# Kernel tuning notes

Measured on AMD Instinct MI355X. Metric: run time of the kernel, lower is better.

## Reference

```python
import jax, jax.numpy as jnp
import numpy as np

NEG_INF = -9e15
ALPHA = 0.2  # LeakyReLU negative slope


def setup_inputs() -> dict:
    key = jax.random.key(0)
    k1, k2, k3, k4 = jax.random.split(key, 4)
    B, N, C_IN, C_OUT, H = 8, 2048, 256, 256, 4
    node_feats = jax.random.normal(k1, (B, N, C_IN), dtype=jnp.float32)
    adj_matrix = jax.random.randint(k2, (B, N, N), 0, 2, dtype=jnp.int32)
    # include self-connections as the docstring expects
    eye = jnp.eye(N, dtype=jnp.int32)[None]
    adj_matrix = jnp.maximum(adj_matrix, eye)
    W = jax.random.normal(k3, (C_OUT, C_IN), dtype=jnp.float32) * (1.414 / np.sqrt(C_IN))
    b = jnp.zeros((C_OUT,), dtype=jnp.float32)
    a = jax.random.normal(k4, (H, 2 * (C_OUT // H)), dtype=jnp.float32) * 0.1
    return {"node_feats": node_feats, "adj_matrix": adj_matrix, "W": W, "b": b, "a": a}


def reference(node_feats, adj_matrix, W, b, a):
    B, N, _ = node_feats.shape
    H, two_c = a.shape
    c = two_c // 2
    # projection: [B, N, H, c]
    f = (jnp.einsum('bni,oi->bno', node_feats, W) + b).reshape(B, N, H, c)
    # attention logit for edge (i, j): leakyrelu(a . [f_i, f_j])
    # decomposes as leakyrelu(s_src[i] + s_dst[j])
    a_src, a_dst = a[:, :c], a[:, c:]
    s_src = jnp.einsum('bnhc,hc->bnh', f, a_src)  # [B, N, H]
    s_dst = jnp.einsum('bnhc,hc->bnh', f, a_dst)  # [B, N, H]
    logits = jax.nn.leaky_relu(s_src[:, :, None, :] + s_dst[:, None, :, :], ALPHA)  # [B,N,N,H]
    logits = jnp.where(adj_matrix[..., None] == 1, logits, NEG_INF)
    probs = jax.nn.softmax(logits, axis=2)  # softmax over source nodes j
    out = jnp.einsum('bijh,bjhc->bihc', probs, f)
    return out.reshape(B, N, H * c)  # concat_heads=True
```

## Files before the change

kernel.cpp:

```cpp
#include <hip/hip_runtime.h>

#define LOG2E 1.4426950408889634f

typedef __attribute__((ext_vector_type(8))) short short8;
typedef __attribute__((ext_vector_type(4))) float f32x4;

union AF { unsigned u[4]; short8 v; };
union BB { uint4 q; short8 v; };

__device__ __forceinline__ unsigned short f2bf(float f) {
  unsigned int u = __float_as_uint(f);
  u = (u + 0x7fffu + ((u >> 16) & 1u)) >> 16;
  return (unsigned short)u;
}

__global__ __launch_bounds__(256) void gat_k1(
    const float* __restrict__ X, const float* __restrict__ W,
    const float* __restrict__ bias, const float* __restrict__ a,
    unsigned short* __restrict__ ft, float* __restrict__ ssrc,
    float* __restrict__ sdst)
{
  __shared__ float Xs[8][128];
  __shared__ float Ws[8][128];
  const int tid = threadIdx.x;
  const int tx = tid & 15, ty = tid >> 4;
  const int m0 = blockIdx.x * 128;
  const int c0 = blockIdx.y * 128;

  float acc[8][8];
#pragma unroll
  for (int r = 0; r < 8; ++r)
#pragma unroll
    for (int j = 0; j < 8; ++j) acc[r][j] = 0.f;

  const int lrow = tid >> 1;
  const int kk0 = (tid & 1) * 4;
  const float* Xp = X + (size_t)(m0 + lrow) * 256 + kk0;
  const float* Wp = W + (size_t)(c0 + lrow) * 256 + kk0;

  for (int kc = 0; kc < 256; kc += 8) {
    float4 xv = *(const float4*)(Xp + kc);
    float4 wv = *(const float4*)(Wp + kc);
    __syncthreads();
    Xs[kk0 + 0][lrow] = xv.x; Xs[kk0 + 1][lrow] = xv.y;
    Xs[kk0 + 2][lrow] = xv.z; Xs[kk0 + 3][lrow] = xv.w;
    Ws[kk0 + 0][lrow] = wv.x; Ws[kk0 + 1][lrow] = wv.y;
    Ws[kk0 + 2][lrow] = wv.z; Ws[kk0 + 3][lrow] = wv.w;
    __syncthreads();
#pragma unroll
    for (int kk = 0; kk < 8; ++kk) {
      float av[8], wv8[8];
#pragma unroll
      for (int r = 0; r < 8; ++r) av[r] = Xs[kk][ty * 8 + r];
#pragma unroll
      for (int j = 0; j < 8; ++j) wv8[j] = Ws[kk][tx * 8 + j];
#pragma unroll
      for (int r = 0; r < 8; ++r)
#pragma unroll
        for (int j = 0; j < 8; ++j) acc[r][j] = fmaf(av[r], wv8[j], acc[r][j]);
    }
  }

  const int b = m0 >> 11;
  const int nloc0 = (m0 & 2047) + ty * 8;
  const int cg0 = c0 + tx * 8;
  const int h = cg0 >> 6;
  const int cb = cg0 & 63;

  float bv[8], av_s[8], av_d[8];
#pragma unroll
  for (int j = 0; j < 8; ++j) {
    bv[j]   = bias[cg0 + j];
    av_s[j] = a[h * 128 + cb + j];
    av_d[j] = a[h * 128 + 64 + cb + j];
  }
#pragma unroll
  for (int r = 0; r < 8; ++r)
#pragma unroll
    for (int j = 0; j < 8; ++j) acc[r][j] += bv[j];

  const int jt = nloc0 >> 4;
  const int ni = nloc0 & 15;
#pragma unroll
  for (int j = 0; j < 8; ++j) {
    unsigned int u[4];
#pragma unroll
    for (int q = 0; q < 4; ++q) {
      unsigned int lo = f2bf(acc[2 * q + 0][j]);
      unsigned int hi = f2bf(acc[2 * q + 1][j]);
      u[q] = lo | (hi << 16);
    }
    size_t off = ((((size_t)b * 128 + jt) * 4 + h) * 64 + (cb + j)) * 16 + ni;
    *(uint4*)(ft + off) = make_uint4(u[0], u[1], u[2], u[3]);
  }

  float sp[8], dp[8];
#pragma unroll
  for (int r = 0; r < 8; ++r) {
    float s = 0.f, d = 0.f;
#pragma unroll
    for (int j = 0; j < 8; ++j) {
      s = fmaf(acc[r][j], av_s[j], s);
      d = fmaf(acc[r][j], av_d[j], d);
    }
    sp[r] = s; dp[r] = d;
  }
#pragma unroll
  for (int off = 1; off < 8; off <<= 1) {
#pragma unroll
    for (int r = 0; r < 8; ++r) {
      sp[r] += __shfl_xor(sp[r], off);
      dp[r] += __shfl_xor(dp[r], off);
    }
  }
  if ((tx & 7) == 0) {
    float* sb = ssrc + ((size_t)b * 4 + h) * 2048 + nloc0;
    float* db = sdst + ((size_t)b * 4 + h) * 2048 + nloc0;
#pragma unroll
    for (int r = 0; r < 8; ++r) { sb[r] = sp[r] * LOG2E; db[r] = dp[r] * LOG2E; }
  }
}

__global__ __launch_bounds__(512, 5) void gat_k2(
    const int* __restrict__ adj, const unsigned short* __restrict__ ft,
    const float* __restrict__ ssrc, const float* __restrict__ sdst,
    float* __restrict__ out)
{
  __shared__ __align__(16) unsigned char lds[37120];
  float* sd = (float*)lds;
  unsigned* Aw = (unsigned*)(lds + 32768);

  const int tid = threadIdx.x;
  const int b = blockIdx.x & 7;
  const int itile = blockIdx.x >> 3;
  const int i0 = itile * 16;
  const int w = tid >> 6;
  const int h = w >> 1;
  const int p = w & 1;
  const int lane = tid & 63;
  const int i_l = lane & 15;
  const int kg = lane >> 4;
  const int shamt = kg * 8;

  const unsigned short* ftb =
      ft + ((((size_t)b * 128 + p * 64 + (kg >> 1)) * 4 + h) * 64 + i_l) * 16 +
      (kg & 1) * 8;

  uint4 A0, A1, A2, A3, B0, B1, B2, B3;
#define LOADB(s, P0_, P1_, P2_, P3_)                               \
  {                                                                \
    const unsigned short* fp_ = ftb + (size_t)(s) * 8192;          \
    P0_ = *(const uint4*)(fp_);                                    \
    P1_ = *(const uint4*)(fp_ + 256);                              \
    P2_ = *(const uint4*)(fp_ + 512);                              \
    P3_ = *(const uint4*)(fp_ + 768);                              \
  }
  LOADB(0, A0, A1, A2, A3)
  LOADB(1, B0, B1, B2, B3)

  {
    const float4* src = (const float4*)(sdst + (size_t)b * 4 * 2048);
    float4* dst = (float4*)sd;
#pragma unroll
    for (int q = 0; q < 4; ++q) dst[tid + q * 512] = src[tid + q * 512];
  }
  {
    const int* abase = adj + (size_t)b * 2048 * 2048 + (size_t)i0 * 2048;
    unsigned short* dst16 = (unsigned short*)Aw;
#pragma unroll
    for (int k = 0; k < 4; ++k) {
      const int idx = k * 512 + tid;
      const int r = idx >> 7;
      const int s16 = idx & 127;
      const int4* ap = (const int4*)(abase + (size_t)r * 2048 + s16 * 16);
      int4 v0 = ap[0], v1 = ap[1], v2 = ap[2], v3 = ap[3];
      int vv[16] = {v0.x, v0.y, v0.z, v0.w, v1.x, v1.y, v1.z, v1.w,
                    v2.x, v2.y, v2.z, v2.w, v3.x, v3.y, v3.z, v3.w};
      unsigned m = 0;
#pragma unroll
      for (int i = 0; i < 16; ++i) m |= (vv[i] ? 1u : 0u) << i;
      dst16[((s16 >> 1) * 17 + r) * 2 + (s16 & 1)] = (unsigned short)m;
    }
  }
  const float si = ssrc[((size_t)b * 4 + h) * 2048 + i0 + i_l];
  const float* sdh = sd + h * 2048 + p * 1024 + kg * 8;

  f32x4 acc0, acc1, acc2, acc3;
#pragma unroll
  for (int q = 0; q < 4; ++q) { acc0[q] = 0.f; acc1[q] = 0.f; acc2[q] = 0.f; acc3[q] = 0.f; }
  float lsumA = 0.f, lsumB = 0.f;

  __syncthreads();

#define LOADM(s, mw_, t0_, t1_)                                    \
  {                                                                \
    mw_ = Aw[(p * 32 + (s)) * 17 + i_l];                           \
    const float* tp_ = sdh + (size_t)(s) * 32;                     \
    t0_ = *(const float4*)tp_;                                     \
    t1_ = *(const float4*)(tp_ + 4);                               \
  }

#define COMPE(mw_, t0_, t1_, af_, lsum_)                           \
  {                                                                \
    const unsigned byte_ = ((mw_) >> shamt) & 0xffu;               \
    float tj_[8] = {t0_.x, t0_.y, t0_.z, t0_.w,                    \
                    t1_.x, t1_.y, t1_.z, t1_.w};                   \
    float e_[8];                                                   \
    _Pragma("unroll")                                              \
    for (int q = 0; q < 8; ++q) {                                  \
      float x_ = si + tj_[q];                                      \
      float y_ = fmaxf(x_, 0.2f * x_);                             \
      float ev_ = __builtin_amdgcn_exp2f(y_);                      \
      e_[q] = (byte_ & (1u << q)) ? ev_ : 0.f;                     \
    }                                                              \
    float s01_ = e_[0] + e_[1], s23_ = e_[2] + e_[3];              \
    float s45_ = e_[4] + e_[5], s67_ = e_[6] + e_[7];              \
    lsum_ += (s01_ + s23_) + (s45_ + s67_);                        \
    _Pragma("unroll")                                              \
    for (int q2 = 0; q2 < 4; ++q2) {                               \
      unsigned r_;                                                 \
      asm("v_cvt_pk_bf16_f32 %0, %1, %2"                           \
          : "=v"(r_) : "v"(e_[2 * q2]), "v"(e_[2 * q2 + 1]));      \
      af_.u[q2] = r_;                                              \
    }                                                              \
  }

#define DOMFMA(af_, P0_, P1_, P2_, P3_)                            \
  {                                                                \
    BB bb_;                                                        \
    bb_.q = P0_;                                                   \
    acc0 = __builtin_amdgcn_mfma_f32_16x16x32_bf16(af_.v, bb_.v, acc0, 0, 0, 0); \
    bb_.q = P1_;                                                   \
    acc1 = __builtin_amdgcn_mfma_f32_16x16x32_bf16(af_.v, bb_.v, acc1, 0, 0, 0); \
    bb_.q = P2_;                                                   \
    acc2 = __builtin_amdgcn_mfma_f32_16x16x32_bf16(af_.v, bb_.v, acc2, 0, 0, 0); \
    bb_.q = P3_;                                                   \
    acc3 = __builtin_amdgcn_mfma_f32_16x16x32_bf16(af_.v, bb_.v, acc3, 0, 0, 0); \
  }

  unsigned mwA, mwB;
  float4 ta0, ta1, tb0, tb1;
  LOADM(0, mwA, ta0, ta1)

  for (int s = 0; s < 32; s += 2) {
    LOADM(s + 1, mwB, tb0, tb1)
    AF afA;
    COMPE(mwA, ta0, ta1, afA, lsumA)
    DOMFMA(afA, A0, A1, A2, A3)
    {
      const int sn = (s + 2 < 32) ? s + 2 : 31;
      LOADB(sn, A0, A1, A2, A3)
    }
    {
      const int sm = (s + 2 < 32) ? s + 2 : 31;
      LOADM(sm, mwA, ta0, ta1)
    }
    AF afB;
    COMPE(mwB, tb0, tb1, afB, lsumB)
    DOMFMA(afB, B0, B1, B2, B3)
    {
      const int sn = (s + 3 < 32) ? s + 3 : 31;
      LOADB(sn, B0, B1, B2, B3)
    }
  }
#undef LOADB
#undef LOADM
#undef COMPE
#undef DOMFMA

  float lsum = lsumA + lsumB;

  float lsum2 = lsum + __shfl_xor(lsum, 16);
  lsum2 += __shfl_xor(lsum2, 32);
  float* ep = (float*)lds;
  float* el = (float*)(lds + 16384);
  __syncthreads();
  if (p == 1) {
#pragma unroll
    for (int r = 0; r < 4; ++r) {
      const int row = kg * 4 + r;
      ep[(h * 16 + row) * 64 + 0  + i_l] = acc0[r];
      ep[(h * 16 + row) * 64 + 16 + i_l] = acc1[r];
      ep[(h * 16 + row) * 64 + 32 + i_l] = acc2[r];
      ep[(h * 16 + row) * 64 + 48 + i_l] = acc3[r];
    }
    if (lane < 16) el[h * 16 + lane] = lsum2;
  }
  __syncthreads();
  if (p == 0) {
    const float L = lsum2 + el[h * 16 + i_l];
    const float rinv = 1.0f / L;
    float* ob = out + ((size_t)(b * 2048 + i0)) * 256 + h * 64;
#pragma unroll
    for (int r = 0; r < 4; ++r) {
      const int row = kg * 4 + r;
      const float ri = __shfl(rinv, row);
      ob[(size_t)row * 256 + 0  + i_l] = (acc0[r] + ep[(h * 16 + row) * 64 + 0  + i_l]) * ri;
      ob[(size_t)row * 256 + 16 + i_l] = (acc1[r] + ep[(h * 16 + row) * 64 + 16 + i_l]) * ri;
      ob[(size_t)row * 256 + 32 + i_l] = (acc2[r] + ep[(h * 16 + row) * 64 + 32 + i_l]) * ri;
      ob[(size_t)row * 256 + 48 + i_l] = (acc3[r] + ep[(h * 16 + row) * 64 + 48 + i_l]) * ri;
    }
  }
}

extern "C" void kernel_launch(void* const* d_in, const int* in_sizes, int n_in,
                              void* d_out, int out_size, void* d_ws, size_t ws_size,
                              hipStream_t stream) {
  const float* X    = (const float*)d_in[0];
  const int*   adj  = (const int*)d_in[1];
  const float* W    = (const float*)d_in[2];
  const float* bias = (const float*)d_in[3];
  const float* a    = (const float*)d_in[4];
  float* out = (float*)d_out;

  unsigned short* ft = (unsigned short*)d_ws;
  float* ssrc = (float*)((char*)d_ws + 8388608);
  float* sdst = ssrc + 8 * 4 * 2048;

  gat_k1<<<dim3(128, 2, 1), 256, 0, stream>>>(X, W, bias, a, ft, ssrc, sdst);
  gat_k2<<<dim3(1024, 1, 1), 512, 0, stream>>>(adj, ft, ssrc, sdst, out);
}
```

Measured before the change: 106.6 us.

## Compute softmax row sums via extra MFMA with ones and simplify loop

The softmax denominator is now taken from a fifth MFMA against a ones vector, replacing the per-lane VALU add tree and the cross-lane shuffles. Because the row sum is built from the bf16-rounded probabilities, it now matches the numerator's rounding. The loop is restructured to use pointer increments and peels the tail steps, which removes the clamped redundant loads of the old version. The launch-bounds occupancy hint is raised from 5 to 6 blocks, trading register headroom (including the new accumulator) for more resident waves.

Measured after the change: 104.6 us. Within noise of the previous version (-1.8%).

```diff
diff --git a/kernel.cpp b/kernel.cpp
--- a/kernel.cpp
+++ b/kernel.cpp
@@ -2,11 +2,10 @@
 
 #define LOG2E 1.4426950408889634f
 
-typedef __attribute__((ext_vector_type(8))) short short8;
+typedef __attribute__((ext_vector_type(8))) short bf16x8;
 typedef __attribute__((ext_vector_type(4))) float f32x4;
 
-union AF { unsigned u[4]; short8 v; };
-union BB { uint4 q; short8 v; };
+union AF { unsigned u[4]; bf16x8 v; };
 
 __device__ __forceinline__ unsigned short f2bf(float f) {
   unsigned int u = __float_as_uint(f);
@@ -121,7 +120,7 @@
   }
 }
 
-__global__ __launch_bounds__(512, 5) void gat_k2(
+__global__ __launch_bounds__(512, 6) void gat_k2(
     const int* __restrict__ adj, const unsigned short* __restrict__ ft,
     const float* __restrict__ ssrc, const float* __restrict__ sdst,
     float* __restrict__ out)
@@ -142,21 +141,14 @@
   const int kg = lane >> 4;
   const int shamt = kg * 8;
 
-  const unsigned short* ftb =
-      ft + ((((size_t)b * 128 + p * 64 + (kg >> 1)) * 4 + h) * 64 + i_l) * 16 +
-      (kg & 1) * 8;
-
-  uint4 A0, A1, A2, A3, B0, B1, B2, B3;
-#define LOADB(s, P0_, P1_, P2_, P3_)                               \
-  {                                                                \
-    const unsigned short* fp_ = ftb + (size_t)(s) * 8192;          \
-    P0_ = *(const uint4*)(fp_);                                    \
-    P1_ = *(const uint4*)(fp_ + 256);                              \
-    P2_ = *(const uint4*)(fp_ + 512);                              \
-    P3_ = *(const uint4*)(fp_ + 768);                              \
-  }
-  LOADB(0, A0, A1, A2, A3)
-  LOADB(1, B0, B1, B2, B3)
+  const bf16x8* fp = (const bf16x8*)ft +
+      ((((size_t)b * 128 + p * 64 + (kg >> 1)) * 4 + h) * 64 + i_l) * 2 +
+      (kg & 1);
+
+  bf16x8 A0 = fp[0], A1 = fp[32], A2 = fp[64], A3 = fp[96];
+  fp += 1024;
+  bf16x8 B0 = fp[0], B1 = fp[32], B2 = fp[64], B3 = fp[96];
+  fp += 1024;
 
   {
     const float4* src = (const float4*)(sdst + (size_t)b * 4 * 2048);
@@ -183,24 +175,22 @@
     }
   }
   const float si = ssrc[((size_t)b * 4 + h) * 2048 + i0 + i_l];
-  const float* sdh = sd + h * 2048 + p * 1024 + kg * 8;
-
-  f32x4 acc0, acc1, acc2, acc3;
-#pragma unroll
-  for (int q = 0; q < 4; ++q) { acc0[q] = 0.f; acc1[q] = 0.f; acc2[q] = 0.f; acc3[q] = 0.f; }
-  float lsumA = 0.f, lsumB = 0.f;
+
+  const unsigned* awp = Aw + (p * 32) * 17 + i_l;
+  const float* sdp = sd + h * 2048 + p * 1024 + kg * 8;
+
+  f32x4 acc0, acc1, acc2, acc3, acc4;
+#pragma unroll
+  for (int q = 0; q < 4; ++q) {
+    acc0[q] = 0.f; acc1[q] = 0.f; acc2[q] = 0.f; acc3[q] = 0.f; acc4[q] = 0.f;
+  }
+  bf16x8 ones;
+#pragma unroll
+  for (int q = 0; q < 8; ++q) ones[q] = (short)0x3F80;
 
   __syncthreads();
 
-#define LOADM(s, mw_, t0_, t1_)                                    \
-  {                                                                \
-    mw_ = Aw[(p * 32 + (s)) * 17 + i_l];                           \
-    const float* tp_ = sdh + (size_t)(s) * 32;                     \
-    t0_ = *(const float4*)tp_;                                     \
-    t1_ = *(const float4*)(tp_ + 4);                               \
-  }
-
-#define COMPE(mw_, t0_, t1_, af_, lsum_)                           \
+#define STEP(mw_, t0_, t1_, F0_, F1_, F2_, F3_)                    \
   {                                                                \
     const unsigned byte_ = ((mw_) >> shamt) & 0xffu;               \
     float tj_[8] = {t0_.x, t0_.y, t0_.z, t0_.w,                    \
@@ -213,9 +203,7 @@
       float ev_ = __builtin_amdgcn_exp2f(y_);                      \
       e_[q] = (byte_ & (1u << q)) ? ev_ : 0.f;                     \
     }                                                              \
-    float s01_ = e_[0] + e_[1], s23_ = e_[2] + e_[3];              \
-    float s45_ = e_[4] + e_[5], s67_ = e_[6] + e_[7];              \
-    lsum_ += (s01_ + s23_) + (s45_ + s67_);                        \
+    AF af_;                                                        \
     _Pragma("unroll")                                              \
     for (int q2 = 0; q2 < 4; ++q2) {                               \
       unsigned r_;                                                 \
@@ -223,55 +211,43 @@
           : "=v"(r_) : "v"(e_[2 * q2]), "v"(e_[2 * q2 + 1]));      \
       af_.u[q2] = r_;                                              \
     }                                                              \
-  }
-
-#define DOMFMA(af_, P0_, P1_, P2_, P3_)                            \
-  {                                                                \
-    BB bb_;                                                        \
-    bb_.q = P0_;                                                   \
-    acc0 = __builtin_amdgcn_mfma_f32_16x16x32_bf16(af_.v, bb_.v, acc0, 0, 0, 0); \
-    bb_.q = P1_;                                                   \
-    acc1 = __builtin_amdgcn_mfma_f32_16x16x32_bf16(af_.v, bb_.v, acc1, 0, 0, 0); \
-    bb_.q = P2_;                                                   \
-    acc2 = __builtin_amdgcn_mfma_f32_16x16x32_bf16(af_.v, bb_.v, acc2, 0, 0, 0); \
-    bb_.q = P3_;                                                   \
-    acc3 = __builtin_amdgcn_mfma_f32_16x16x32_bf16(af_.v, bb_.v, acc3, 0, 0, 0); \
+    acc0 = __builtin_amdgcn_mfma_f32_16x16x32_bf16(af_.v, F0_, acc0, 0, 0, 0); \
+    acc1 = __builtin_amdgcn_mfma_f32_16x16x32_bf16(af_.v, F1_, acc1, 0, 0, 0); \
+    acc2 = __builtin_amdgcn_mfma_f32_16x16x32_bf16(af_.v, F2_, acc2, 0, 0, 0); \
+    acc3 = __builtin_amdgcn_mfma_f32_16x16x32_bf16(af_.v, F3_, acc3, 0, 0, 0); \
+    acc4 = __builtin_amdgcn_mfma_f32_16x16x32_bf16(af_.v, ones, acc4, 0, 0, 0); \
   }
 
   unsigned mwA, mwB;
   float4 ta0, ta1, tb0, tb1;
-  LOADM(0, mwA, ta0, ta1)
-
-  for (int s = 0; s < 32; s += 2) {
-    LOADM(s + 1, mwB, tb0, tb1)
-    AF afA;
-    COMPE(mwA, ta0, ta1, afA, lsumA)
-    DOMFMA(afA, A0, A1, A2, A3)
-    {
-      const int sn = (s + 2 < 32) ? s + 2 : 31;
-      LOADB(sn, A0, A1, A2, A3)
-    }
-    {
-      const int sm = (s + 2 < 32) ? s + 2 : 31;
-      LOADM(sm, mwA, ta0, ta1)
-    }
-    AF afB;
-    COMPE(mwB, tb0, tb1, afB, lsumB)
-    DOMFMA(afB, B0, B1, B2, B3)
-    {
-      const int sn = (s + 3 < 32) ? s + 3 : 31;
-      LOADB(sn, B0, B1, B2, B3)
-    }
-  }
-#undef LOADB
-#undef LOADM
-#undef COMPE
-#undef DOMFMA
-
-  float lsum = lsumA + lsumB;
-
-  float lsum2 = lsum + __shfl_xor(lsum, 16);
-  lsum2 += __shfl_xor(lsum2, 32);
+  mwA = awp[0];
+  ta0 = *(const float4*)sdp;
+  ta1 = *(const float4*)(sdp + 4);
+  awp += 17; sdp += 32;
+
+  for (int s = 0; s < 30; s += 2) {
+    mwB = awp[0];
+    tb0 = *(const float4*)sdp;
+    tb1 = *(const float4*)(sdp + 4);
+    awp += 17; sdp += 32;
+    STEP(mwA, ta0, ta1, A0, A1, A2, A3)
+    A0 = fp[0]; A1 = fp[32]; A2 = fp[64]; A3 = fp[96];
+    fp += 1024;
+    mwA = awp[0];
+    ta0 = *(const float4*)sdp;
+    ta1 = *(const float4*)(sdp + 4);
+    awp += 17; sdp += 32;
+    STEP(mwB, tb0, tb1, B0, B1, B2, B3)
+    B0 = fp[0]; B1 = fp[32]; B2 = fp[64]; B3 = fp[96];
+    fp += 1024;
+  }
+  mwB = awp[0];
+  tb0 = *(const float4*)sdp;
+  tb1 = *(const float4*)(sdp + 4);
+  STEP(mwA, ta0, ta1, A0, A1, A2, A3)
+  STEP(mwB, tb0, tb1, B0, B1, B2, B3)
+#undef STEP
+
   float* ep = (float*)lds;
   float* el = (float*)(lds + 16384);
   __syncthreads();
@@ -284,17 +260,19 @@
       ep[(h * 16 + row) * 64 + 32 + i_l] = acc2[r];
       ep[(h * 16 + row) * 64 + 48 + i_l] = acc3[r];
     }
-    if (lane < 16) el[h * 16 + lane] = lsum2;
+    if (i_l == 0) {
+#pragma unroll
+      for (int r = 0; r < 4; ++r) el[h * 16 + kg * 4 + r] = acc4[r];
+    }
   }
   __syncthreads();
   if (p == 0) {
-    const float L = lsum2 + el[h * 16 + i_l];
-    const float rinv = 1.0f / L;
     float* ob = out + ((size_t)(b * 2048 + i0)) * 256 + h * 64;
 #pragma unroll
     for (int r = 0; r < 4; ++r) {
       const int row = kg * 4 + r;
-      const float ri = __shfl(rinv, row);
+      const float L = acc4[r] + el[h * 16 + row];
+      const float ri = 1.0f / L;
       ob[(size_t)row * 256 + 0  + i_l] = (acc0[r] + ep[(h * 16 + row) * 64 + 0  + i_l]) * ri;
       ob[(size_t)row * 256 + 16 + i_l] = (acc1[r] + ep[(h * 16 + row) * 64 + 16 + i_l]) * ri;
       ob[(size_t)row * 256 + 32 + i_l] = (acc2[r] + ep[(h * 16 + row) * 64 + 32 + i_l]) * ri;
```
